# Kernel tuning notes

Measured on AMD Instinct MI355X. Metric: run time of the kernel, lower is better.

## Reference

```python
import math
import jax, jax.numpy as jnp
import numpy as np

B, C, H, W = 16, 128, 128, 128  # width == dim required by nn.LayerNorm(dim) on (b,c,h,w)
HEADS, DIM_HEAD = 8, 32
INNER = HEADS * DIM_HEAD


def _ln_last(x, g, b, eps=1e-5):
    # torch nn.LayerNorm over the LAST axis (here: width), biased variance
    mu = x.mean(-1, keepdims=True)
    var = x.var(-1, keepdims=True)
    return (x - mu) * jax.lax.rsqrt(var + eps) * g + b


def setup_inputs() -> dict:
    key = jax.random.key(0)
    k0, k1, k2 = jax.random.split(key, 3)
    return {
        "fmap": jax.random.normal(k0, (B, C, H, W), jnp.float32),
        "ln0_g": jnp.ones((C,), jnp.float32),
        "ln0_b": jnp.zeros((C,), jnp.float32),
        "w_qkv": jax.random.normal(k1, (3 * INNER, C), jnp.float32) * 0.05,
        "w_out": jax.random.normal(k2, (C, INNER), jnp.float32) * 0.05,
        "ln1_g": jnp.ones((C,), jnp.float32),
        "ln1_b": jnp.zeros((C,), jnp.float32),
    }


def reference(fmap, ln0_g, ln0_b, w_qkv, w_out, ln1_g, ln1_b):
    b, c, x, y = fmap.shape
    n = x * y
    scale = DIM_HEAD ** -0.5

    fm = _ln_last(fmap, ln0_g, ln0_b)
    # 1x1 conv (no bias) == channel matmul
    qkv = jnp.einsum('bcxy,oc->boxy', fm, w_qkv)  # (b, 3*inner, x, y)
    q, k, v = jnp.split(qkv, 3, axis=1)

    def to_heads(t):
        # b (h c) x y -> (b h) (x y) c
        return t.reshape(b, HEADS, DIM_HEAD, n).transpose(0, 1, 3, 2).reshape(b * HEADS, n, DIM_HEAD)

    q, k, v = map(to_heads, (q, k, v))

    q = jax.nn.softmax(q, axis=-1) * scale
    k = jax.nn.softmax(k, axis=-2)
    # l2norm(v) along feature dim (F.normalize, eps=1e-12)
    v = v / jnp.clip(jnp.linalg.norm(v, axis=-1, keepdims=True), 1e-12)
    inv = 1.0 / math.sqrt(n)
    k = k * inv
    v = v * inv

    context = jnp.einsum('bnd,bne->bde', k, v)   # small (d=32, e=32) context
    out = jnp.einsum('bnd,bde->bne', q, context)

    # (b h) (x y) d -> b (h d) x y
    out = out.reshape(b, HEADS, n, DIM_HEAD).transpose(0, 1, 3, 2).reshape(b, INNER, x, y)
    out = jax.nn.gelu(out, approximate=False)  # torch nn.GELU default (erf)
    out = jnp.einsum('bcxy,oc->boxy', out, w_out)  # 1x1 conv, no bias
    return _ln_last(out, ln1_g, ln1_b)
```

## Files before the change

kernel.cpp:

```cpp
#include <hip/hip_runtime.h>
#include <math.h>

#define OFF_MU    0u
#define OFF_RSTD  262144u
#define OFF_CTXA  524288u
#define OFF_CTXP  2686976u
#define OFF_WSPL  2883584u
#define OFF_WQSPL 2981888u
#define OFF_WOSPL 3031040u

typedef __attribute__((ext_vector_type(8))) short bf16x8;
typedef __attribute__((ext_vector_type(4))) float f32x4;

__device__ __forceinline__ void split3(float v, unsigned& h, unsigned& m, unsigned& l) {
  unsigned u = __float_as_uint(v);
  float r1 = v - __uint_as_float(u & 0xffff0000u);
  unsigned u1 = __float_as_uint(r1);
  float r2 = r1 - __uint_as_float(u1 & 0xffff0000u);
  h = u >> 16; m = u1 >> 16; l = __float_as_uint(r2) >> 16;
}

__device__ __forceinline__ f32x4 mfma6(const bf16x8& A0, const bf16x8& A1, const bf16x8& A2,
                                       const bf16x8& B0, const bf16x8& B1, const bf16x8& B2,
                                       f32x4 c) {
  c = __builtin_amdgcn_mfma_f32_16x16x32_bf16(A0, B0, c, 0, 0, 0);
  c = __builtin_amdgcn_mfma_f32_16x16x32_bf16(A0, B1, c, 0, 0, 0);
  c = __builtin_amdgcn_mfma_f32_16x16x32_bf16(A1, B0, c, 0, 0, 0);
  c = __builtin_amdgcn_mfma_f32_16x16x32_bf16(A0, B2, c, 0, 0, 0);
  c = __builtin_amdgcn_mfma_f32_16x16x32_bf16(A1, B1, c, 0, 0, 0);
  c = __builtin_amdgcn_mfma_f32_16x16x32_bf16(A2, B0, c, 0, 0, 0);
  return c;
}

__global__ void prep_kernel(const float* __restrict__ wqkv,
                            const float* __restrict__ wout,
                            float* __restrict__ ws) {
  int idx = blockIdx.x * 256 + threadIdx.x;
  float v;
  unsigned short* wp;
  unsigned plane, slot;
  if (idx < 65536) {
    int row = idx >> 7, c = idx & 127;
    int blk = row >> 7, ol = row & 127;
    int hh = (ol >> 5) & 1;
    int src = ((ol & 64) ? 512 : 256) + (2 * blk + hh) * 32 + (ol & 31);
    v = wqkv[src * 128 + c];
    wp = (unsigned short*)(ws + OFF_WSPL);
    plane = 65536; slot = (unsigned)idx;
  } else if (idx < 98304) {
    int j = idx - 65536;
    v = wqkv[j];
    wp = (unsigned short*)(ws + OFF_WQSPL);
    plane = 32768; slot = (unsigned)j;
  } else {
    int j = idx - 98304;
    int o = j >> 8, k = j & 255;
    int cp = (k & 0xE0) | (((k >> 2) & 1) << 4) | (((k >> 3) & 3) << 2) | (k & 3);
    v = wout[o * 256 + cp];
    wp = (unsigned short*)(ws + OFF_WOSPL);
    plane = 32768; slot = (unsigned)j;
  }
  unsigned h, m, l;
  split3(v, h, m, l);
  wp[slot]             = (unsigned short)h;
  wp[plane + slot]     = (unsigned short)m;
  wp[2 * plane + slot] = (unsigned short)l;
}

__global__ void ln0_stats_kernel(const float* __restrict__ fmap,
                                 float* __restrict__ ws) {
  const int wid = threadIdx.x >> 6, lane = threadIdx.x & 63;
  const int row = blockIdx.x * 4 + wid;
  const float* p = fmap + (size_t)row * 128;
  float a0 = p[lane], a1 = p[lane + 64];
  double s = (double)a0 + (double)a1;
  double q = (double)a0 * a0 + (double)a1 * a1;
  #pragma unroll
  for (int off = 32; off; off >>= 1) {
    s += __shfl_xor(s, off);
    q += __shfl_xor(q, off);
  }
  if (lane == 0) {
    double mu = s * (1.0 / 128.0);
    double var = q * (1.0 / 128.0) - mu * mu;
    ws[OFF_MU + row] = (float)mu;
    ws[OFF_RSTD + row] = (float)(1.0 / sqrt(var + 1e-5));
  }
}

__launch_bounds__(512, 4)
__global__ void kv_ctx_kernel(const float* __restrict__ fmap,
                              const float* __restrict__ g0,
                              const float* __restrict__ b0,
                              float* __restrict__ ws) {
  __shared__ float sm[13888];
  const int x = blockIdx.x, b = blockIdx.y, t = threadIdx.x;
  const int wave = t >> 6, lane = t & 63;
  const int ln = lane & 15, kb = lane >> 4;
  const int or2 = wave >> 1, yc = wave & 1;
  const int dt = lane >> 3, et = lane & 7;
  const int xg = x >> 3;

  float* pb  = sm;
  float* vb  = sm + 2304;
  float* vss = sm + 4608;
  float* ser = sm + 4864;
  float* rnS = sm + 5120;
  float* red = sm + 5184;
  float* pls = sm + 5184;
  float* muS = sm + 13376;
  float* rsS = sm + 13504;
  float* g0S = sm + 13632;
  float* b0S = sm + 13760;
  float* fmS = sm;

  if (t < 128) {
    muS[t] = ws[OFF_MU + (unsigned)((b * 128 + t) * 128 + x)];
    rsS[t] = ws[OFF_RSTD + (unsigned)((b * 128 + t) * 128 + x)];
  } else if (t < 256) g0S[t - 128] = g0[t - 128];
  else if (t < 384) b0S[t - 256] = b0[t - 256];

  const unsigned short* wspl = (const unsigned short*)(ws + OFF_WSPL);

  for (int blk = 0; blk < 4; ++blk) {
    f32x4 acc[2][4];
    #pragma unroll
    for (int i = 0; i < 2; ++i)
      #pragma unroll
      for (int j = 0; j < 4; ++j) acc[i][j] = (f32x4){0.f, 0.f, 0.f, 0.f};

    for (int cc = 0; cc < 4; ++cc) {
      bf16x8 af[2][3];
      #pragma unroll
      for (int ot = 0; ot < 2; ++ot)
        #pragma unroll
        for (int p = 0; p < 3; ++p)
          af[ot][p] = *(const bf16x8*)(wspl + p * 65536 +
              ((blk * 128 + or2 * 32 + ot * 16 + ln) * 128 + cc * 32 + kb * 8));

      __syncthreads();
      #pragma unroll
      for (int it = 0; it < 2; ++it) {
        int idx4 = it * 512 + t;
        int c = idx4 >> 5, y4 = (idx4 & 31) * 4;
        int cg = cc * 32 + c;
        const float4 r = *(const float4*)(fmap + (((size_t)(b * 128 + cg)) * 128 + x) * 128 + y4);
        float mu = muS[cg], rs = rsS[cg];
        float4 g = *(const float4*)(g0S + y4);
        float4 be = *(const float4*)(b0S + y4);
        float4 o;
        o.x = (r.x - mu) * rs * g.x + be.x;
        o.y = (r.y - mu) * rs * g.y + be.y;
        o.z = (r.z - mu) * rs * g.z + be.z;
        o.w = (r.w - mu) * rs * g.w + be.w;
        *(float4*)(fmS + c * 128 + y4) = o;
      }
      __syncthreads();
      {
        const int ty = t & 127, cg = t >> 7;
        unsigned int d0[4], d1[4], d2[4];
        #pragma unroll
        for (int jj = 0; jj < 4; ++jj) {
          unsigned int h[2], m[2], l[2];
          #pragma unroll
          for (int e = 0; e < 2; ++e) {
            float v = fmS[(cg * 8 + jj * 2 + e) * 128 + ty];
            split3(v, h[e], m[e], l[e]);
          }
          d0[jj] = h[0] | (h[1] << 16);
          d1[jj] = m[0] | (m[1] << 16);
          d2[jj] = l[0] | (l[1] << 16);
        }
        float* pp = pls + ty * 20 + cg * 4;
        *reinterpret_cast<uint4*>(pp)        = make_uint4(d0[0], d0[1], d0[2], d0[3]);
        *reinterpret_cast<uint4*>(pp + 2560) = make_uint4(d1[0], d1[1], d1[2], d1[3]);
        *reinterpret_cast<uint4*>(pp + 5120) = make_uint4(d2[0], d2[1], d2[2], d2[3]);
      }
      __syncthreads();
      #pragma unroll
      for (int yt = 0; yt < 4; ++yt) {
        const float* bp = pls + ((yc * 4 + yt) * 16 + ln) * 20 + kb * 4;
        bf16x8 B0 = *(const bf16x8*)(bp);
        bf16x8 B1 = *(const bf16x8*)(bp + 2560);
        bf16x8 B2 = *(const bf16x8*)(bp + 5120);
        #pragma unroll
        for (int ot = 0; ot < 2; ++ot)
          acc[ot][yt] = mfma6(af[ot][0], af[ot][1], af[ot][2], B0, B1, B2, acc[ot][yt]);
      }
    }

    for (int hh = 0; hh < 2; ++hh) {
      float u[16], se[4];
      #pragma unroll
      for (int i = 0; i < 16; ++i) u[i] = 0.0f;
      se[0] = se[1] = se[2] = se[3] = 0.0f;

      for (int hf = 0; hf < 2; ++hf) {
        if (wave == hh * 2 + hf) {
          #pragma unroll
          for (int ot = 0; ot < 2; ++ot)
            #pragma unroll
            for (int yt = 0; yt < 4; ++yt) {
              f32x4 a = acc[ot][yt];
              float4 p;
              p.x = __expf(a[0]); p.y = __expf(a[1]);
              p.z = __expf(a[2]); p.w = __expf(a[3]);
              *(float4*)(pb + (yt * 16 + ln) * 36 + ot * 16 + kb * 4) = p;
            }
        }
        if (wave == 4 + hh * 2 + hf) {
          #pragma unroll
          for (int yt = 0; yt < 4; ++yt) {
            f32x4 a0 = acc[0][yt], a1 = acc[1][yt];
            int yl = yt * 16 + ln;
            *(float4*)(vb + yl * 36 + kb * 4)      = make_float4(a0[0], a0[1], a0[2], a0[3]);
            *(float4*)(vb + yl * 36 + 16 + kb * 4) = make_float4(a1[0], a1[1], a1[2], a1[3]);
            float s = a0[0] * a0[0] + a0[1] * a0[1] + a0[2] * a0[2] + a0[3] * a0[3]
                    + a1[0] * a1[0] + a1[1] * a1[1] + a1[2] * a1[2] + a1[3] * a1[3];
            vss[kb * 64 + yl] = s;
          }
        }
        __syncthreads();
        if (t < 64) {
          float s2 = vss[t] + vss[64 + t] + vss[128 + t] + vss[192 + t];
          rnS[t] = 1.0f / fmaxf(sqrtf(s2), 1e-12f);
        }
        __syncthreads();
        #pragma unroll 2
        for (int yy = 0; yy < 8; ++yy) {
          int y = wave * 8 + yy;
          const float4 p = *(const float4*)(pb + y * 36 + dt * 4);
          float4 v = *(const float4*)(vb + y * 36 + et * 4);
          float rn = rnS[y];
          v.x *= rn; v.y *= rn; v.z *= rn; v.w *= rn;
          se[0] += p.x; se[1] += p.y; se[2] += p.z; se[3] += p.w;
          u[0]  = fmaf(p.x, v.x, u[0]);  u[1]  = fmaf(p.x, v.y, u[1]);
          u[2]  = fmaf(p.x, v.z, u[2]);  u[3]  = fmaf(p.x, v.w, u[3]);
          u[4]  = fmaf(p.y, v.x, u[4]);  u[5]  = fmaf(p.y, v.y, u[5]);
          u[6]  = fmaf(p.y, v.z, u[6]);  u[7]  = fmaf(p.y, v.w, u[7]);
          u[8]  = fmaf(p.z, v.x, u[8]);  u[9]  = fmaf(p.z, v.y, u[9]);
          u[10] = fmaf(p.z, v.z, u[10]); u[11] = fmaf(p.z, v.w, u[11]);
          u[12] = fmaf(p.w, v.x, u[12]); u[13] = fmaf(p.w, v.y, u[13]);
          u[14] = fmaf(p.w, v.z, u[14]); u[15] = fmaf(p.w, v.w, u[15]);
        }
        __syncthreads();
      }
      *(float4*)(red + t * 16 + 0)  = make_float4(u[0], u[1], u[2], u[3]);
      *(float4*)(red + t * 16 + 4)  = make_float4(u[4], u[5], u[6], u[7]);
      *(float4*)(red + t * 16 + 8)  = make_float4(u[8], u[9], u[10], u[11]);
      *(float4*)(red + t * 16 + 12) = make_float4(u[12], u[13], u[14], u[15]);
      if (et == 0)
        *(float4*)(ser + (wave * 8 + dt) * 4) = make_float4(se[0], se[1], se[2], se[3]);
      __syncthreads();
      {
        const int tile = t >> 3;
        const int i0 = (t & 7) * 2;
        float s0 = 0.0f, s1 = 0.0f;
        #pragma unroll
        for (int w = 0; w < 8; ++w) {
          s0 += red[(w * 64 + tile) * 16 + i0];
          s1 += red[(w * 64 + tile) * 16 + i0 + 1];
        }
        const int d = (tile >> 3) * 4 + (i0 >> 2);
        const int e = (tile & 7) * 4 + (i0 & 3);
        float* ca = ws + OFF_CTXA + ((size_t)(b * 8 + blk * 2 + hh) * 16 + xg) * 1056;
        atomicAdd(ca + d * 32 + e, s0);
        atomicAdd(ca + d * 32 + e + 1, s1);
        if (t < 32) {
          float ss = 0.0f;
          #pragma unroll
          for (int w = 0; w < 8; ++w) ss += ser[(w * 8 + (t >> 2)) * 4 + (t & 3)];
          atomicAdd(ca + 1024 + t, ss);
        }
      }
    }
  }
}

__global__ void ctx_reduce_kernel(float* __restrict__ ws) {
  __shared__ float sume[32];
  const int bh = blockIdx.x, t = threadIdx.x;
  const float* ca = ws + OFF_CTXA + (size_t)bh * 16 * 1056;
  if (t < 32) {
    double a = 0.0;
    #pragma unroll
    for (int xg = 0; xg < 16; ++xg) a += ca[xg * 1056 + 1024 + t];
    sume[t] = (float)a;
  }
  __syncthreads();
  const double sb = (1.0 / 16384.0) * 0.17677669529663688;
  unsigned short* cp = (unsigned short*)(ws + OFF_CTXP) + (size_t)bh * 3072;
  #pragma unroll
  for (int i = 0; i < 4; ++i) {
    int de = t + 256 * i;
    int d = de >> 5, e = de & 31;
    double a = 0.0;
    #pragma unroll
    for (int xg = 0; xg < 16; ++xg) a += ca[xg * 1056 + de];
    float v = (float)(a * sb / (double)sume[d]);
    int k = ((d >> 2) & 3) * 8 + ((d >> 4) & 1) * 4 + (d & 3);
    unsigned h, m, l;
    split3(v, h, m, l);
    cp[e * 32 + k]        = (unsigned short)h;
    cp[1024 + e * 32 + k] = (unsigned short)m;
    cp[2048 + e * 32 + k] = (unsigned short)l;
  }
}

__launch_bounds__(512, 4)
__global__ void final_kernel(const float* __restrict__ fmap,
                             const float* __restrict__ g0,
                             const float* __restrict__ b0,
                             const float* __restrict__ g1,
                             const float* __restrict__ b1,
                             const float* __restrict__ ws,
                             float* __restrict__ out) {
  __shared__ float sm[14592];
  const int x = blockIdx.x, b = blockIdx.y, t = threadIdx.x;
  const int wave = t >> 6, lane = t & 63;
  const int ln = lane & 15, kb = lane >> 4;
  const int or2 = wave >> 1, yc = wave & 1;

  float* fmS = sm;
  float* pls = sm + 4096;
  float* gel = sm;
  float* muS = sm + 13824;
  float* rsS = sm + 13952;
  float* g0S = sm + 14080;
  float* b0S = sm + 14208;
  float* lnm = sm + 14336;
  float* lnr = sm + 14464;

  if (t < 128) {
    muS[t] = ws[OFF_MU + (unsigned)((b * 128 + t) * 128 + x)];
    rsS[t] = ws[OFF_RSTD + (unsigned)((b * 128 + t) * 128 + x)];
  } else if (t < 256) g0S[t - 128] = g0[t - 128];
  else if (t < 384) b0S[t - 256] = b0[t - 256];

  const unsigned short* wqspl = (const unsigned short*)(ws + OFF_WQSPL);
  const unsigned short* wospl = (const unsigned short*)(ws + OFF_WOSPL);
  const unsigned short* ctxp  = (const unsigned short*)(ws + OFF_CTXP);

  f32x4 oacc[2][4];
  #pragma unroll
  for (int i = 0; i < 2; ++i)
    #pragma unroll
    for (int j = 0; j < 4; ++j) oacc[i][j] = (f32x4){0.f, 0.f, 0.f, 0.f};

  for (int qblk = 0; qblk < 2; ++qblk) {
    f32x4 qacc[2][4];
    #pragma unroll
    for (int i = 0; i < 2; ++i)
      #pragma unroll
      for (int j = 0; j < 4; ++j) qacc[i][j] = (f32x4){0.f, 0.f, 0.f, 0.f};

    for (int cc = 0; cc < 4; ++cc) {
      bf16x8 af[2][3];
      #pragma unroll
      for (int ot = 0; ot < 2; ++ot)
        #pragma unroll
        for (int p = 0; p < 3; ++p)
          af[ot][p] = *(const bf16x8*)(wqspl + p * 32768 +
              ((qblk * 128 + or2 * 32 + ot * 16 + ln) * 128 + cc * 32 + kb * 8));

      __syncthreads();
      #pragma unroll
      for (int it = 0; it < 2; ++it) {
        int idx4 = it * 512 + t;
        int c = idx4 >> 5, y4 = (idx4 & 31) * 4;
        int cg = cc * 32 + c;
        const float4 r = *(const float4*)(fmap + (((size_t)(b * 128 + cg)) * 128 + x) * 128 + y4);
        float mu = muS[cg], rs = rsS[cg];
        float4 g = *(const float4*)(g0S + y4);
        float4 be = *(const float4*)(b0S + y4);
        float4 o;
        o.x = (r.x - mu) * rs * g.x + be.x;
        o.y = (r.y - mu) * rs * g.y + be.y;
        o.z = (r.z - mu) * rs * g.z + be.z;
        o.w = (r.w - mu) * rs * g.w + be.w;
        *(float4*)(fmS + c * 128 + y4) = o;
      }
      __syncthreads();
      {
        const int ty = t & 127, cg = t >> 7;
        unsigned int d0[4], d1[4], d2[4];
        #pragma unroll
        for (int jj = 0; jj < 4; ++jj) {
          unsigned int h[2], m[2], l[2];
          #pragma unroll
          for (int e = 0; e < 2; ++e) {
            float v = fmS[(cg * 8 + jj * 2 + e) * 128 + ty];
            split3(v, h[e], m[e], l[e]);
          }
          d0[jj] = h[0] | (h[1] << 16);
          d1[jj] = m[0] | (m[1] << 16);
          d2[jj] = l[0] | (l[1] << 16);
        }
        float* pp = pls + ty * 20 + cg * 4;
        *reinterpret_cast<uint4*>(pp)        = make_uint4(d0[0], d0[1], d0[2], d0[3]);
        *reinterpret_cast<uint4*>(pp + 2560) = make_uint4(d1[0], d1[1], d1[2], d1[3]);
        *reinterpret_cast<uint4*>(pp + 5120) = make_uint4(d2[0], d2[1], d2[2], d2[3]);
      }
      __syncthreads();
      #pragma unroll
      for (int yt = 0; yt < 4; ++yt) {
        const float* bp = pls + ((yc * 4 + yt) * 16 + ln) * 20 + kb * 4;
        bf16x8 B0 = *(const bf16x8*)(bp);
        bf16x8 B1 = *(const bf16x8*)(bp + 2560);
        bf16x8 B2 = *(const bf16x8*)(bp + 5120);
        #pragma unroll
        for (int ot = 0; ot < 2; ++ot)
          qacc[ot][yt] = mfma6(af[ot][0], af[ot][1], af[ot][2], B0, B1, B2, qacc[ot][yt]);
      }
    }

    float rssum[4];
    bf16x8 pf0[4], pf1[4], pf2[4];
    #pragma unroll
    for (int yt = 0; yt < 4; ++yt) {
      float pv[8];
      #pragma unroll
      for (int ot = 0; ot < 2; ++ot)
        #pragma unroll
        for (int r = 0; r < 4; ++r)
          pv[ot * 4 + r] = __expf(qacc[ot][yt][r]);
      float ps = ((pv[0] + pv[1]) + (pv[2] + pv[3])) + ((pv[4] + pv[5]) + (pv[6] + pv[7]));
      ps += __shfl_xor(ps, 16);
      ps += __shfl_xor(ps, 32);
      rssum[yt] = 1.0f / ps;
      unsigned wh[4], wm[4], wl[4];
      #pragma unroll
      for (int j = 0; j < 4; ++j) {
        unsigned h0, m0, l0, h1, m1, l1;
        split3(pv[2 * j], h0, m0, l0);
        split3(pv[2 * j + 1], h1, m1, l1);
        wh[j] = h0 | (h1 << 16);
        wm[j] = m0 | (m1 << 16);
        wl[j] = l0 | (l1 << 16);
      }
      uint4 uh = make_uint4(wh[0], wh[1], wh[2], wh[3]);
      uint4 um = make_uint4(wm[0], wm[1], wm[2], wm[3]);
      uint4 ul = make_uint4(wl[0], wl[1], wl[2], wl[3]);
      pf0[yt] = *(const bf16x8*)&uh;
      pf1[yt] = *(const bf16x8*)&um;
      pf2[yt] = *(const bf16x8*)&ul;
    }

    f32x4 ge[2][4];
    const unsigned short* chp = ctxp + (size_t)(b * 8 + qblk * 4 + or2) * 3072;
    #pragma unroll
    for (int ot = 0; ot < 2; ++ot) {
      bf16x8 aq0 = *(const bf16x8*)(chp +        (ot * 16 + ln) * 32 + kb * 8);
      bf16x8 aq1 = *(const bf16x8*)(chp + 1024 + (ot * 16 + ln) * 32 + kb * 8);
      bf16x8 aq2 = *(const bf16x8*)(chp + 2048 + (ot * 16 + ln) * 32 + kb * 8);
      #pragma unroll
      for (int yt = 0; yt < 4; ++yt) {
        f32x4 c = (f32x4){0.f, 0.f, 0.f, 0.f};
        ge[ot][yt] = mfma6(aq0, aq1, aq2, pf0[yt], pf1[yt], pf2[yt], c);
      }
    }

    #pragma unroll
    for (int ot = 0; ot < 2; ++ot)
      #pragma unroll
      for (int yt = 0; yt < 4; ++yt)
        #pragma unroll
        for (int r = 0; r < 4; ++r) {
          float v = ge[ot][yt][r] * rssum[yt];
          ge[ot][yt][r] = 0.5f * v * (1.0f + erff(v * 0.70710678118654752f));
        }

    for (int ph = 0; ph < 2; ++ph) {
      __syncthreads();
      if ((or2 >> 1) == ph) {
        const int c16 = (or2 & 1) * 16;
        #pragma unroll
        for (int yt = 0; yt < 4; ++yt) {
          float* grow = gel + ((yc * 4 + yt) * 16 + ln) * 36 + c16 + kb * 4;
          #pragma unroll
          for (int ot = 0; ot < 2; ++ot) {
            unsigned h0, m0, l0, h1, m1, l1, h2, m2, l2, h3, m3, l3;
            split3(ge[ot][yt][0], h0, m0, l0);
            split3(ge[ot][yt][1], h1, m1, l1);
            split3(ge[ot][yt][2], h2, m2, l2);
            split3(ge[ot][yt][3], h3, m3, l3);
            *(uint2*)(grow + ot * 2)        = make_uint2(h0 | (h1 << 16), h2 | (h3 << 16));
            *(uint2*)(grow + 4608 + ot * 2) = make_uint2(m0 | (m1 << 16), m2 | (m3 << 16));
            *(uint2*)(grow + 9216 + ot * 2) = make_uint2(l0 | (l1 << 16), l2 | (l3 << 16));
          }
        }
      }
      __syncthreads();
      #pragma unroll
      for (int kc = 0; kc < 2; ++kc) {
        bf16x8 ao[2][3];
        #pragma unroll
        for (int ot = 0; ot < 2; ++ot)
          #pragma unroll
          for (int p = 0; p < 3; ++p)
            ao[ot][p] = *(const bf16x8*)(wospl + p * 32768 +
                ((or2 * 32 + ot * 16 + ln) * 256 + qblk * 128 + ph * 64 + kc * 32 + kb * 8));
        #pragma unroll
        for (int yt = 0; yt < 4; ++yt) {
          const float* bp = gel + ((yc * 4 + yt) * 16 + ln) * 36 + kc * 16 + kb * 4;
          bf16x8 B0 = *(const bf16x8*)(bp);
          bf16x8 B1 = *(const bf16x8*)(bp + 4608);
          bf16x8 B2 = *(const bf16x8*)(bp + 9216);
          #pragma unroll
          for (int ot = 0; ot < 2; ++ot)
            oacc[ot][yt] = mfma6(ao[ot][0], ao[ot][1], ao[ot][2], B0, B1, B2, oacc[ot][yt]);
        }
      }
    }
  }

  __syncthreads();
  float* red_s = sm;
  float* red_q = sm + 4096;
  #pragma unroll
  for (int ot = 0; ot < 2; ++ot)
    #pragma unroll
    for (int r = 0; r < 4; ++r) {
      int o = or2 * 32 + ot * 16 + kb * 4 + r;
      float s = 0.0f, q = 0.0f;
      #pragma unroll
      for (int yt = 0; yt < 4; ++yt) { float v = oacc[ot][yt][r]; s += v; q = fmaf(v, v, q); }
      red_s[o * 32 + yc * 16 + ln] = s;
      red_q[o * 32 + yc * 16 + ln] = q;
    }
  __syncthreads();
  if (t < 128) {
    double s = 0.0, q = 0.0;
    #pragma unroll
    for (int i = 0; i < 32; ++i) { s += red_s[t * 32 + i]; q += red_q[t * 32 + i]; }
    double mu = s * (1.0 / 128.0);
    double var = q * (1.0 / 128.0) - mu * mu;
    lnm[t] = (float)mu;
    lnr[t] = (float)(1.0 / sqrt(var + 1e-5));
  }
  __syncthreads();
  float g1v[4], b1v[4];
  #pragma unroll
  for (int yt = 0; yt < 4; ++yt) {
    int y = (yc * 4 + yt) * 16 + ln;
    g1v[yt] = g1[y]; b1v[yt] = b1[y];
  }
  #pragma unroll
  for (int ot = 0; ot < 2; ++ot)
    #pragma unroll
    for (int r = 0; r < 4; ++r) {
      int o = or2 * 32 + ot * 16 + kb * 4 + r;
      float mu = lnm[o], rs = lnr[o];
      #pragma unroll
      for (int yt = 0; yt < 4; ++yt) {
        int y = (yc * 4 + yt) * 16 + ln;
        out[(((size_t)(b * 128 + o)) * 128 + x) * 128 + y] =
            (oacc[ot][yt][r] - mu) * rs * g1v[yt] + b1v[yt];
      }
    }
}

extern "C" void kernel_launch(void* const* d_in, const int* in_sizes, int n_in,
                              void* d_out, int out_size, void* d_ws, size_t ws_size,
                              hipStream_t stream) {
  const float* fmap = (const float*)d_in[0];
  const float* g0   = (const float*)d_in[1];
  const float* b0   = (const float*)d_in[2];
  const float* wqkv = (const float*)d_in[3];
  const float* wout = (const float*)d_in[4];
  const float* g1   = (const float*)d_in[5];
  const float* b1   = (const float*)d_in[6];
  float* ws  = (float*)d_ws;
  float* out = (float*)d_out;

  hipMemsetAsync((char*)d_ws + (size_t)OFF_CTXA * 4, 0, (size_t)2162688 * 4, stream);
  prep_kernel<<<512, 256, 0, stream>>>(wqkv, wout, ws);
  ln0_stats_kernel<<<65536, 256, 0, stream>>>(fmap, ws);
  kv_ctx_kernel<<<dim3(128, 16), 512, 0, stream>>>(fmap, g0, b0, ws);
  ctx_reduce_kernel<<<128, 256, 0, stream>>>(ws);
  final_kernel<<<dim3(128, 16), 512, 0, stream>>>(fmap, g0, b0, g1, b1, ws, out);
}
```

Measured before the change: 1.043 ms.

## Fuse LayerNorm0 stats into kv_ctx kernel and interleave q-context MFMA with softmax

Removes the separate ln0_stats kernel launch and computes the per-row mean and rstd inside kv_ctx_kernel. Each block reads its own 128 rows of fmap as float4 and reduces them across 4 lanes, then writes the stats to workspace for the final kernel to use. The output path of the final kernel is also restructured so the context MFMA and GELU run per y-tile right after that tile's exp/split. This drops the pf0/pf1/pf2 register arrays to cut register pressure. The trade-off is an extra fmap read in the kv kernel instead of a separate pass, and an asm barrier used to keep offset reuse.

```diff
diff --git a/kernel.cpp b/kernel.cpp
--- a/kernel.cpp
+++ b/kernel.cpp
@@ -67,27 +67,6 @@
   wp[2 * plane + slot] = (unsigned short)l;
 }
 
-__global__ void ln0_stats_kernel(const float* __restrict__ fmap,
-                                 float* __restrict__ ws) {
-  const int wid = threadIdx.x >> 6, lane = threadIdx.x & 63;
-  const int row = blockIdx.x * 4 + wid;
-  const float* p = fmap + (size_t)row * 128;
-  float a0 = p[lane], a1 = p[lane + 64];
-  double s = (double)a0 + (double)a1;
-  double q = (double)a0 * a0 + (double)a1 * a1;
-  #pragma unroll
-  for (int off = 32; off; off >>= 1) {
-    s += __shfl_xor(s, off);
-    q += __shfl_xor(q, off);
-  }
-  if (lane == 0) {
-    double mu = s * (1.0 / 128.0);
-    double var = q * (1.0 / 128.0) - mu * mu;
-    ws[OFF_MU + row] = (float)mu;
-    ws[OFF_RSTD + row] = (float)(1.0 / sqrt(var + 1e-5));
-  }
-}
-
 __launch_bounds__(512, 4)
 __global__ void kv_ctx_kernel(const float* __restrict__ fmap,
                               const float* __restrict__ g0,
@@ -114,11 +93,29 @@
   float* b0S = sm + 13760;
   float* fmS = sm;
 
-  if (t < 128) {
-    muS[t] = ws[OFF_MU + (unsigned)((b * 128 + t) * 128 + x)];
-    rsS[t] = ws[OFF_RSTD + (unsigned)((b * 128 + t) * 128 + x)];
-  } else if (t < 256) g0S[t - 128] = g0[t - 128];
-  else if (t < 384) b0S[t - 256] = b0[t - 256];
+  {
+    const int r = t >> 2, q = t & 3;
+    const float* p = fmap + (((size_t)(b * 128 + r)) * 128 + x) * 128 + q * 32;
+    double s = 0.0, qq = 0.0;
+    #pragma unroll
+    for (int i = 0; i < 8; ++i) {
+      float4 v4 = *(const float4*)(p + i * 4);
+      s  += (double)v4.x + (double)v4.y + (double)v4.z + (double)v4.w;
+      qq += (double)v4.x * v4.x + (double)v4.y * v4.y
+          + (double)v4.z * v4.z + (double)v4.w * v4.w;
+    }
+    s += __shfl_xor(s, 1); qq += __shfl_xor(qq, 1);
+    s += __shfl_xor(s, 2); qq += __shfl_xor(qq, 2);
+    if (q == 0) {
+      double mu = s * (1.0 / 128.0);
+      double var = qq * (1.0 / 128.0) - mu * mu;
+      float muf = (float)mu, rsf = (float)(1.0 / sqrt(var + 1e-5));
+      muS[r] = muf; rsS[r] = rsf;
+      ws[OFF_MU + (unsigned)((b * 128 + r) * 128 + x)] = muf;
+      ws[OFF_RSTD + (unsigned)((b * 128 + r) * 128 + x)] = rsf;
+    }
+  }
+  if (t < 128) { g0S[t] = g0[t]; b0S[t] = b0[t]; }
 
   const unsigned short* wspl = (const unsigned short*)(ws + OFF_WSPL);
 
@@ -414,8 +411,8 @@
       }
     }
 
-    float rssum[4];
-    bf16x8 pf0[4], pf1[4], pf2[4];
+    f32x4 ge[2][4];
+    const unsigned short* chp = ctxp + (size_t)(b * 8 + qblk * 4 + or2) * 3072;
     #pragma unroll
     for (int yt = 0; yt < 4; ++yt) {
       float pv[8];
@@ -427,7 +424,7 @@
       float ps = ((pv[0] + pv[1]) + (pv[2] + pv[3])) + ((pv[4] + pv[5]) + (pv[6] + pv[7]));
       ps += __shfl_xor(ps, 16);
       ps += __shfl_xor(ps, 32);
-      rssum[yt] = 1.0f / ps;
+      const float rs = 1.0f / ps;
       unsigned wh[4], wm[4], wl[4];
       #pragma unroll
       for (int j = 0; j < 4; ++j) {
@@ -441,34 +438,24 @@
       uint4 uh = make_uint4(wh[0], wh[1], wh[2], wh[3]);
       uint4 um = make_uint4(wm[0], wm[1], wm[2], wm[3]);
       uint4 ul = make_uint4(wl[0], wl[1], wl[2], wl[3]);
-      pf0[yt] = *(const bf16x8*)&uh;
-      pf1[yt] = *(const bf16x8*)&um;
-      pf2[yt] = *(const bf16x8*)&ul;
-    }
-
-    f32x4 ge[2][4];
-    const unsigned short* chp = ctxp + (size_t)(b * 8 + qblk * 4 + or2) * 3072;
-    #pragma unroll
-    for (int ot = 0; ot < 2; ++ot) {
-      bf16x8 aq0 = *(const bf16x8*)(chp +        (ot * 16 + ln) * 32 + kb * 8);
-      bf16x8 aq1 = *(const bf16x8*)(chp + 1024 + (ot * 16 + ln) * 32 + kb * 8);
-      bf16x8 aq2 = *(const bf16x8*)(chp + 2048 + (ot * 16 + ln) * 32 + kb * 8);
-      #pragma unroll
-      for (int yt = 0; yt < 4; ++yt) {
-        f32x4 c = (f32x4){0.f, 0.f, 0.f, 0.f};
-        ge[ot][yt] = mfma6(aq0, aq1, aq2, pf0[yt], pf1[yt], pf2[yt], c);
-      }
-    }
-
-    #pragma unroll
-    for (int ot = 0; ot < 2; ++ot)
-      #pragma unroll
-      for (int yt = 0; yt < 4; ++yt)
+      bf16x8 P0 = *(const bf16x8*)&uh;
+      bf16x8 P1 = *(const bf16x8*)&um;
+      bf16x8 P2 = *(const bf16x8*)&ul;
+      unsigned off = (unsigned)((0 * 16 + ln) * 32 + kb * 8);
+      asm volatile("" : "+v"(off));
+      #pragma unroll
+      for (int ot = 0; ot < 2; ++ot) {
+        bf16x8 aq0 = *(const bf16x8*)(chp +        off + ot * 512);
+        bf16x8 aq1 = *(const bf16x8*)(chp + 1024 + off + ot * 512);
+        bf16x8 aq2 = *(const bf16x8*)(chp + 2048 + off + ot * 512);
+        f32x4 g = mfma6(aq0, aq1, aq2, P0, P1, P2, (f32x4){0.f, 0.f, 0.f, 0.f});
         #pragma unroll
         for (int r = 0; r < 4; ++r) {
-          float v = ge[ot][yt][r] * rssum[yt];
+          float v = g[r] * rs;
           ge[ot][yt][r] = 0.5f * v * (1.0f + erff(v * 0.70710678118654752f));
         }
+      }
+    }
 
     for (int ph = 0; ph < 2; ++ph) {
       __syncthreads();
@@ -575,7 +562,6 @@
 
   hipMemsetAsync((char*)d_ws + (size_t)OFF_CTXA * 4, 0, (size_t)2162688 * 4, stream);
   prep_kernel<<<512, 256, 0, stream>>>(wqkv, wout, ws);
-  ln0_stats_kernel<<<65536, 256, 0, stream>>>(fmap, ws);
   kv_ctx_kernel<<<dim3(128, 16), 512, 0, stream>>>(fmap, g0, b0, ws);
   ctx_reduce_kernel<<<128, 256, 0, stream>>>(ws);
   final_kernel<<<dim3(128, 16), 512, 0, stream>>>(fmap, g0, b0, g1, b1, ws, out);
```

New measurement: 1.043 ms. No clear change (-0.0%).
